# Optimization experiments

Hardware: AMD Instinct MI355X
Metric: run time of the kernel (lower is better)

Reference implementation:

```python
import jax, jax.numpy as jnp
import numpy as np

EPS = 1e-8
MIN_VAL = -1e7  # module default min_val=-10000000.0


def _div_safe(n, d):
    return n / jnp.maximum(d, EPS)


def _cosine_pairwise(v1, v2):
    # v1: (B,L1,H), v2: (B,L2,H) -> (B,L1,L2)
    n1 = jnp.linalg.norm(v1, axis=2, keepdims=True)
    n2 = jnp.linalg.norm(v2, axis=2, keepdims=True)
    a = jnp.einsum('bik,bjk->bij', v1, v2)
    return _div_safe(a, n1 * jnp.swapaxes(n2, 1, 2))


def _masked_max(v, mask, axis, keepdims=False):
    rep = jnp.where(mask > 0, v, MIN_VAL)
    val = jnp.max(rep, axis=axis, keepdims=keepdims)
    m = jnp.max(jnp.broadcast_to(mask, v.shape), axis=axis, keepdims=keepdims)
    return val * m


def _masked_mean(v, mask, axis, keepdims=False):
    s = jnp.sum(v * mask, axis=axis, keepdims=keepdims)
    c = jnp.sum(jnp.broadcast_to(mask, v.shape), axis=axis, keepdims=keepdims)
    return _div_safe(s, c)


def _cos_sim(a, b, axis):
    # torch F.cosine_similarity semantics: dot / (max(|a|,eps)*max(|b|,eps))
    dot = jnp.sum(a * b, axis=axis)
    na = jnp.maximum(jnp.linalg.norm(a, axis=axis), EPS)
    nb = jnp.maximum(jnp.linalg.norm(b, axis=axis), EPS)
    return dot / (na * nb)


def _mpm(v1, v2, w):
    # v1, v2: (B,L,H); w: (P,H) -> ((B,L,1), (B,L,P))
    mv1 = _cos_sim(v1, v2, 2)[..., None]
    v1w = w[None, None] * v1[:, :, None, :]  # (B,L,P,H)
    v2w = w[None, None] * v2[:, :, None, :]
    return mv1, _cos_sim(v1w, v2w, 3)


def _mpm_pairwise(v1, v2, w):
    # v1: (B,L1,H), v2: (B,L2,H), w: (P,H) -> (B,L1,L2,P)
    v1w = w[None, :, None, :] * v1[:, None, :, :]  # (B,P,L1,H)
    v2w = w[None, :, None, :] * v2[:, None, :, :]  # (B,P,L2,H)
    n1 = jnp.linalg.norm(v1w, axis=3, keepdims=True)
    n2 = jnp.linalg.norm(v2w, axis=3, keepdims=True)
    n = jnp.einsum('bpik,bpjk->bpij', v1w, v2w)
    d = n1 * jnp.swapaxes(n2, 2, 3)
    return jnp.transpose(_div_safe(n, d), (0, 2, 3, 1))


def setup_inputs() -> dict:
    key = jax.random.key(0)
    ks = jax.random.split(key, 8)
    B, L, H, P = 32, 128, 100, 20
    return {
        'context_p': jax.random.normal(ks[0], (B, L, H), dtype=jnp.float32),
        'mask_p': jax.random.randint(ks[1], (B, L), 0, 2, dtype=jnp.int32),
        'context_h': jax.random.normal(ks[2], (B, L, H), dtype=jnp.float32),
        'mask_h': jax.random.randint(ks[3], (B, L), 0, 2, dtype=jnp.int32),
        'w0': jax.random.uniform(ks[4], (P, H), dtype=jnp.float32),
        'w1': jax.random.uniform(ks[5], (P, H), dtype=jnp.float32),
        'w2': jax.random.uniform(ks[6], (P, H), dtype=jnp.float32),
        'w3': jax.random.uniform(ks[7], (P, H), dtype=jnp.float32),
    }


def reference(context_p, mask_p, context_h, mask_h, w0, w1, w2, w3):
    mask_p = mask_p.astype(jnp.float32)
    mask_h = mask_h.astype(jnp.float32)
    B, Lp, H = context_p.shape
    Lh = context_h.shape[1]

    mask_p_h = mask_p[:, :, None] * mask_h[:, None, :]   # (B,Lp,Lh)
    mask_h_p = jnp.swapaxes(mask_p_h, 1, 2)              # (B,Lh,Lp)
    cp = context_p * mask_p[..., None]
    ch = context_h * mask_h[..., None]

    # --- pairwise cosine + masked max/mean pooling ---
    cos = _cosine_pairwise(cp, ch)                        # (B,Lp,Lh)
    cosT = jnp.swapaxes(cos, 1, 2)
    cos_max_p = _masked_max(cos, mask_p_h, 2, True)
    cos_mean_p = _masked_mean(cos, mask_p_h, 2, True)
    cos_max_h = _masked_max(cosT, mask_h_p, 2, True)
    cos_mean_h = _masked_mean(cosT, mask_h_p, 2, True)

    # --- full match (is_forward=True: last real token) ---
    idx_p = jnp.clip(jnp.sum(mask_p, 1).astype(jnp.int32) - 1, 0)[:, None, None]
    idx_h = jnp.clip(jnp.sum(mask_h, 1).astype(jnp.int32) - 1, 0)[:, None, None]
    cp_last = jnp.take_along_axis(cp, jnp.broadcast_to(idx_p, (B, 1, H)), axis=1)
    ch_last = jnp.take_along_axis(ch, jnp.broadcast_to(idx_h, (B, 1, H)), axis=1)
    mv_p_f1, mv_p_fP = _mpm(cp, jnp.broadcast_to(ch_last, (B, Lp, H)), w0)
    mv_h_f1, mv_h_fP = _mpm(ch, jnp.broadcast_to(cp_last, (B, Lh, H)), w0)

    # --- maxpool match ---
    mv_max = _mpm_pairwise(cp, ch, w1)                    # (B,Lp,Lh,P)
    mv_p_max = _masked_max(mv_max, mask_p_h[..., None], 2)
    mv_p_mean = _masked_mean(mv_max, mask_p_h[..., None], 2)
    mv_maxT = jnp.transpose(mv_max, (0, 2, 1, 3))
    mv_h_max = _masked_max(mv_maxT, mask_h_p[..., None], 2)
    mv_h_mean = _masked_mean(mv_maxT, mask_h_p[..., None], 2)

    # --- attentive match (mean) ---
    att_mean_h = _div_safe(jnp.einsum('bij,bjh->bih', cos, ch),
                           jnp.sum(cos, 2, keepdims=True))
    att_mean_p = _div_safe(jnp.einsum('bij,bih->bjh', cos, cp),
                           jnp.swapaxes(jnp.sum(cos, 1, keepdims=True), 1, 2))
    mv_p_am1, mv_p_amP = _mpm(cp, att_mean_h, w2)
    mv_h_am1, mv_h_amP = _mpm(ch, att_mean_p, w2)

    # --- max-attentive match ---
    att_h = ch[:, None, :, :] * cos[:, :, :, None]        # (B,Lp,Lh,H)
    att_p_t = cp[:, None, :, :] * cosT[:, :, :, None]     # (B,Lh,Lp,H) == att_p.permute(0,2,1,3)
    att_max_h = _masked_max(att_h, mask_p_h[..., None], 2)
    att_max_p = _masked_max(att_p_t, mask_h_p[..., None], 2)
    mv_p_ax1, mv_p_axP = _mpm(cp, att_max_h, w3)
    mv_h_ax1, mv_h_axP = _mpm(ch, att_max_p, w3)

    mv_p = jnp.concatenate([cos_max_p, cos_mean_p, mv_p_f1, mv_p_fP,
                            mv_p_max, mv_p_mean, mv_p_am1, mv_p_amP,
                            mv_p_ax1, mv_p_axP], axis=2)
    mv_h = jnp.concatenate([cos_max_h, cos_mean_h, mv_h_f1, mv_h_fP,
                            mv_h_max, mv_h_mean, mv_h_am1, mv_h_amP,
                            mv_h_ax1, mv_h_axP], axis=2)
    return mv_p, mv_h
```

## Files before the change

### kernel.cpp

```cpp
#include <hip/hip_runtime.h>
#include <math.h>


namespace {
constexpr int B = 32;
constexpr int L = 128;
constexpr int H = 100;
constexpr int P = 20;
constexpr int C = 105;
constexpr int TI = 8;
constexpr float EPSF = 1e-8f;
constexpr float MINV = -1e7f;
}

typedef unsigned short u16;
typedef unsigned int u32;
typedef short sh8 __attribute__((ext_vector_type(8)));
typedef float f4 __attribute__((ext_vector_type(4)));

__device__ __forceinline__ u16 f2bf(float f) {
    u32 u = __float_as_uint(f);
    u += 0x7FFFu + ((u >> 16) & 1u);
    return (u16)(u >> 16);
}
__device__ __forceinline__ float bf2f(u32 h) {
    return __uint_as_float(h << 16);
}

__global__ void k_prep(const float* __restrict__ ctx_p, const int* __restrict__ mask_p,
                       const float* __restrict__ ctx_h, const int* __restrict__ mask_h,
                       const float* __restrict__ w1,
                       float* __restrict__ cp, float* __restrict__ ch,
                       u16* __restrict__ cpb, u16* __restrict__ chb,
                       float* __restrict__ np_, float* __restrict__ nh_,
                       float* __restrict__ nwp, float* __restrict__ nwh)
{
    const int b = blockIdx.y, i = blockIdx.x, side = blockIdx.z, t = threadIdx.x;
    const float* ctx = side ? ctx_h : ctx_p;
    const int*  mask = side ? mask_h : mask_p;
    float* dst  = side ? ch  : cp;
    u16*   dstb = side ? chb : cpb;
    float* nrm  = side ? nh_ : np_;
    float* nw   = side ? nwh : nwp;

    const int row = b * L + i;
    __shared__ __align__(16) float sv2[H];
    const float m = (float)mask[row];
    float v = 0.f;
    if (t < H) {
        v = ctx[row * H + t] * m;
        dst[row * H + t] = v;
        sv2[t] = v * v;
    }
    dstb[row * 128 + t] = f2bf(v);
    __syncthreads();

    const int w = t >> 6, ln = t & 63;
    int g = -1, seg = 0;
    if (w == 0) { if (ln < 60) { g = ln / 5; seg = ln % 5; } }
    else        { if (ln < 45) { g = 12 + ln / 5; seg = ln % 5; } }
    if (g >= 0) {
        const float4* v4 = (const float4*)sv2;
        float acc = 0.f;
        if (g < P) {
            const float4* w4 = (const float4*)(w1 + g * H);
            #pragma unroll
            for (int k = seg * 5; k < seg * 5 + 5; ++k) {
                float4 wv_ = w4[k], s = v4[k];
                acc += wv_.x * wv_.x * s.x + wv_.y * wv_.y * s.y +
                       wv_.z * wv_.z * s.z + wv_.w * wv_.w * s.w;
            }
        } else {
            #pragma unroll
            for (int k = seg * 5; k < seg * 5 + 5; ++k) {
                float4 s = v4[k];
                acc += s.x + s.y + s.z + s.w;
            }
        }
        float a1 = __shfl(acc, ln + 1), a2 = __shfl(acc, ln + 2);
        float a3 = __shfl(acc, ln + 3), a4 = __shfl(acc, ln + 4);
        if (seg == 0) {
            float s = acc + a1 + a2 + a3 + a4;
            if (g < P) nw[row * P + g] = sqrtf(s);
            else       nrm[row] = sqrtf(s);
        }
    }
}

__global__ __launch_bounds__(256) void
k_pair_mfma(const u16* __restrict__ Ab, const u16* __restrict__ Bb,
            const float* __restrict__ w1,
            const float* __restrict__ nwA, const float* __restrict__ nwB,
            const float* __restrict__ np_, const float* __restrict__ nh_,
            const int* __restrict__ maskA, const int* __restrict__ maskB,
            float* __restrict__ outP, float* __restrict__ outH,
            float* __restrict__ cosM, float* __restrict__ cosT,
            float* __restrict__ scP, float* __restrict__ scH)
{
    const int p = blockIdx.x, b = blockIdx.y, t = threadIdx.x;
    const bool is_cos = (p == P);
    __shared__ __align__(16) u16 sB[128 * 136];
    __shared__ float snwA[128], snwB[128], smA[128], smB[128];
    __shared__ float pJmax[128], pJsum[128], pJall[128];
    __shared__ float pImax[4][128], pIsum[4][128], pIall[4][128];
    __shared__ float sRed[4];

    if (t < 128) {
        snwA[t] = is_cos ? np_[b * L + t] : nwA[(b * L + t) * P + p];
        snwB[t] = is_cos ? nh_[b * L + t] : nwB[(b * L + t) * P + p];
        smA[t] = (float)maskA[b * L + t];
        smB[t] = (float)maskB[b * L + t];
    }
    __syncthreads();

    if (t < 64) {
        float a0 = smB[t], a1 = smB[t + 64];
        float mx = fmaxf(a0, a1), sm = a0 + a1;
        for (int d = 1; d < 64; d <<= 1) {
            mx = fmaxf(mx, __shfl_xor(mx, d));
            sm += __shfl_xor(sm, d);
        }
        if (t == 0) { sRed[2] = mx; sRed[3] = sm; }
    } else if (t < 128) {
        const int l = t - 64;
        float a0 = smA[l], a1 = smA[l + 64];
        float mx = fmaxf(a0, a1), sm = a0 + a1;
        for (int d = 1; d < 64; d <<= 1) {
            mx = fmaxf(mx, __shfl_xor(mx, d));
            sm += __shfl_xor(sm, d);
        }
        if (l == 0) { sRed[0] = mx; sRed[1] = sm; }
    }

    {
        const uint4* src = (const uint4*)(Bb + (size_t)b * L * 128);
        #pragma unroll
        for (int it = 0; it < 8; ++it) {
            int idx = it * 256 + t;
            int row = idx >> 4, kc = (idx & 15) * 8;
            uint4 v = src[idx];
            *(uint4*)&sB[row * 136 + kc] = v;
        }
    }
    __syncthreads();

    const int wave = t >> 6, lane = t & 63;
    const int m = lane & 15, q = lane >> 4;

    float swv[4][8];
    #pragma unroll
    for (int ks = 0; ks < 4; ++ks)
        #pragma unroll
        for (int e = 0; e < 8; ++e) {
            int k = ks * 32 + q * 8 + e;
            if (is_cos) swv[ks][e] = (k < H) ? 1.f : 0.f;
            else {
                float w = (k < H) ? w1[p * H + k] : 0.f;
                swv[ks][e] = w * w;
            }
        }

    f4 acc[2][8];
    #pragma unroll
    for (int rt = 0; rt < 2; ++rt)
        #pragma unroll
        for (int ct = 0; ct < 8; ++ct)
            acc[rt][ct] = (f4){0.f, 0.f, 0.f, 0.f};

    const uint4* gA0 = (const uint4*)(Ab + (size_t)(b * L + wave * 32 + m) * 128);
    const uint4* gA1 = (const uint4*)(Ab + (size_t)(b * L + wave * 32 + 16 + m) * 128);

    #pragma unroll
    for (int ks = 0; ks < 4; ++ks) {
        uint4 va0 = gA0[ks * 4 + q];
        uint4 va1 = gA1[ks * 4 + q];
        sh8 a0, a1;
        {
            u32 vs0[4] = {va0.x, va0.y, va0.z, va0.w};
            u32 vs1[4] = {va1.x, va1.y, va1.z, va1.w};
            u32 r0[4], r1[4];
            #pragma unroll
            for (int e = 0; e < 4; ++e) {
                float f0 = bf2f(vs0[e] & 0xffffu) * swv[ks][2 * e];
                float f1 = bf2f(vs0[e] >> 16) * swv[ks][2 * e + 1];
                r0[e] = (u32)f2bf(f0) | ((u32)f2bf(f1) << 16);
                float g0 = bf2f(vs1[e] & 0xffffu) * swv[ks][2 * e];
                float g1 = bf2f(vs1[e] >> 16) * swv[ks][2 * e + 1];
                r1[e] = (u32)f2bf(g0) | ((u32)f2bf(g1) << 16);
            }
            uint4 o0 = {r0[0], r0[1], r0[2], r0[3]};
            uint4 o1 = {r1[0], r1[1], r1[2], r1[3]};
            a0 = __builtin_bit_cast(sh8, o0);
            a1 = __builtin_bit_cast(sh8, o1);
        }
        const int ko = ks * 32 + q * 8;
        #pragma unroll
        for (int ct = 0; ct < 8; ++ct) {
            sh8 bb = *(const sh8*)&sB[(ct * 16 + m) * 136 + ko];
            acc[0][ct] = __builtin_amdgcn_mfma_f32_16x16x32_bf16(a0, bb, acc[0][ct], 0, 0, 0);
            acc[1][ct] = __builtin_amdgcn_mfma_f32_16x16x32_bf16(a1, bb, acc[1][ct], 0, 0, 0);
        }
    }

    float nB[8], mBv[8], imax[8], isum[8], iall[8];
    #pragma unroll
    for (int ct = 0; ct < 8; ++ct) {
        const int j = ct * 16 + m;
        nB[ct] = snwB[j]; mBv[ct] = smB[j];
        imax[ct] = MINV; isum[ct] = 0.f; iall[ct] = 0.f;
    }
    #pragma unroll
    for (int rt = 0; rt < 2; ++rt) {
        #pragma unroll
        for (int reg = 0; reg < 4; ++reg) {
            const int i = wave * 32 + rt * 16 + q * 4 + reg;
            const float na = snwA[i];
            const float ma = smA[i];
            float jmax = MINV, jsum = 0.f, jall = 0.f;
            #pragma unroll
            for (int ct = 0; ct < 8; ++ct) {
                float v = acc[rt][ct][reg] *
                          __builtin_amdgcn_rcpf(fmaxf(na * nB[ct], EPSF));
                if (is_cos) {
                    const int j = ct * 16 + m;
                    cosM[((size_t)b * L + i) * L + j] = v;
                    cosT[((size_t)b * L + j) * L + i] = v;
                    jall += v;
                    iall[ct] += v;
                }
                jmax = fmaxf(jmax, mBv[ct] > 0.f ? v : MINV);
                jsum += mBv[ct] > 0.f ? v : 0.f;
                imax[ct] = fmaxf(imax[ct], ma > 0.f ? v : MINV);
                isum[ct] += ma > 0.f ? v : 0.f;
            }
            for (int d = 1; d < 16; d <<= 1) {
                jmax = fmaxf(jmax, __shfl_xor(jmax, d));
                jsum += __shfl_xor(jsum, d);
                if (is_cos) jall += __shfl_xor(jall, d);
            }
            if (m == 0) { pJmax[i] = jmax; pJsum[i] = jsum; if (is_cos) pJall[i] = jall; }
        }
    }
    #pragma unroll
    for (int ct = 0; ct < 8; ++ct) {
        float mx = imax[ct], sm = isum[ct], al = iall[ct];
        mx = fmaxf(mx, __shfl_xor(mx, 16)); sm += __shfl_xor(sm, 16);
        mx = fmaxf(mx, __shfl_xor(mx, 32)); sm += __shfl_xor(sm, 32);
        if (is_cos) { al += __shfl_xor(al, 16); al += __shfl_xor(al, 32); }
        if (q == 0) {
            const int j = ct * 16 + m;
            pImax[wave][j] = mx; pIsum[wave][j] = sm;
            if (is_cos) pIall[wave][j] = al;
        }
    }
    __syncthreads();

    if (t < 128) {
        const int i = t;
        const int co0 = is_cos ? 0 : 23 + p;
        const int co1 = is_cos ? 1 : 43 + p;
        const float ma = smA[i];
        const float mm = ma * sRed[2];
        const float cnt = ma * sRed[3];
        float* orow = outP + ((size_t)b * L + i) * C;
        orow[co0] = pJmax[i] * mm;
        orow[co1] = ma * pJsum[i] / fmaxf(cnt, EPSF);

        const float mb = smB[i];
        const float hmax = fmaxf(fmaxf(pImax[0][i], pImax[1][i]),
                                 fmaxf(pImax[2][i], pImax[3][i]));
        const float hsum = pIsum[0][i] + pIsum[1][i] + pIsum[2][i] + pIsum[3][i];
        float* hrow = outH + ((size_t)b * L + i) * C;
        hrow[co0] = hmax * mb * sRed[0];
        hrow[co1] = mb * hsum / fmaxf(mb * sRed[1], EPSF);

        if (is_cos) {
            scP[b * L + i] = pJall[i];
            scH[b * L + i] = pIall[0][i] + pIall[1][i] + pIall[2][i] + pIall[3][i];
        }
    }
}

__global__ __launch_bounds__(256, 3) void
k_side_t(const float* __restrict__ cp, const float* __restrict__ ch,
         const u16* __restrict__ cpb, const u16* __restrict__ chb,
         const float* __restrict__ cosM, const float* __restrict__ cosT,
         const float* __restrict__ scP, const float* __restrict__ scH,
         const int* __restrict__ mask_p, const int* __restrict__ mask_h,
         const float* __restrict__ w0, const float* __restrict__ w2,
         const float* __restrict__ w3, float* __restrict__ out)
{
    const int tile = blockIdx.x, b = blockIdx.y, side = blockIdx.z, t = threadIdx.x;
    const int i0 = tile * TI;
    const float* A   = side ? ch : cp;
    const float* Bv  = side ? cp : ch;
    const u16*  Bvb  = side ? cpb : chb;
    const int* maskA = side ? mask_h : mask_p;
    const int* maskB = side ? mask_p : mask_h;
    const float* cosSrc = side ? cosT : cosM;
    const float* scArr  = side ? scH : scP;
    float* outBase = out + ((size_t)side * B * L + (size_t)b * L) * C;

    __shared__ __align__(16) u16  sBvC[128 * 128];
    __shared__ float scosC[TI][128];
    __shared__ __align__(16) float sa[TI][H];
    __shared__ __align__(16) float sam[TI][H];
    __shared__ __align__(16) float sax[TI][H];
    __shared__ __align__(16) float sl[H];
    __shared__ u16 cidx[128];
    __shared__ int snv;

    const int wv = t >> 6, ln = t & 63;

    if (wv == 0) {
        int m0 = maskB[b * L + ln], m1 = maskB[b * L + 64 + ln];
        unsigned long long b0 = __ballot(m0 > 0);
        unsigned long long b1 = __ballot(m1 > 0);
        unsigned long long pre = (1ull << ln) - 1ull;
        int n0 = __popcll(b0);
        if (m0 > 0) cidx[__popcll(b0 & pre)] = (u16)ln;
        if (m1 > 0) cidx[n0 + __popcll(b1 & pre)] = (u16)(64 + ln);
        if (ln == 0) snv = n0 + __popcll(b1);
    } else if (wv >= 2) {
        for (int x = t - 128; x < TI * 128; x += 128) {
            int il = x >> 7, k = x & 127;
            if (k < H) sa[il][k] = A[((size_t)b * L + i0 + il) * H + k];
        }
    }
    __syncthreads();
    const int nv = snv;

    {
        const uint4* src = (const uint4*)(Bvb + (size_t)b * L * 128);
        uint4* dst = (uint4*)sBvC;
        for (int c = t; c < nv * 16; c += 256) {
            int jj = c >> 4, cc = c & 15;
            dst[c] = src[(int)cidx[jj] * 16 + cc];
        }
        for (int x = t; x < TI * 128; x += 256) {
            int il = x >> 7, jj = x & 127;
            if (jj < nv)
                scosC[il][jj] = cosSrc[((size_t)b * L + i0 + il) * L + cidx[jj]];
        }
        if (wv == 1) {
            int last = nv - 1; if (last < 0) last = 0;
            const float* lr = Bv + ((size_t)b * L + last) * H;
            sl[ln] = lr[ln];
            if (ln + 64 < H) sl[ln + 64] = lr[ln + 64];
        }
    }
    __syncthreads();

    #pragma unroll
    for (int pass = 0; pass < 2; ++pass) {
        const int il = wv + pass * 4;
        const int gi = i0 + il;
        if (ln < 50) {
            const float mA = (float)maskA[b * L + gi];
            const float sc = scArr[b * L + gi];
            float am0 = 0.f, am1 = 0.f, ax0 = MINV, ax1 = MINV;
            const u32* bp = (const u32*)sBvC + ln;
            const float* cr = scosC[il];
            #pragma unroll 4
            for (int jj = 0; jj < nv; ++jj) {
                u32 pk = bp[jj * 64];
                float cj = cr[jj];
                float v0 = cj * __uint_as_float(pk << 16);
                float v1 = cj * __uint_as_float(pk & 0xffff0000u);
                am0 += v0; am1 += v1;
                ax0 = fmaxf(ax0, v0); ax1 = fmaxf(ax1, v1);
            }
            const float rs = __builtin_amdgcn_rcpf(fmaxf(sc, EPSF));
            const float mm = (nv > 0) ? mA : 0.f;
            sam[il][2 * ln] = am0 * rs; sam[il][2 * ln + 1] = am1 * rs;
            sax[il][2 * ln] = ax0 * mm; sax[il][2 * ln + 1] = ax1 * mm;
        }
    }
    __syncthreads();

    for (int task = t; task < TI * 63; task += 256) {
        const int il = task / 63, c = task - il * 63;
        float* orow = outBase + (size_t)(i0 + il) * C;
        const float4* a4 = (const float4*)sa[il];
        if (c < 60) {
            const int grp = c / 20, p = c - grp * 20;
            const float* wrow = (grp == 0 ? w0 : grp == 1 ? w2 : w3) + p * H;
            const float* oth = grp == 0 ? sl : grp == 1 ? sam[il] : sax[il];
            const float4* w4 = (const float4*)wrow;
            const float4* o4 = (const float4*)oth;
            float d = 0.f, na = 0.f, nb = 0.f;
            #pragma unroll 5
            for (int k = 0; k < H / 4; ++k) {
                float4 w = w4[k], a = a4[k], o = o4[k];
                float ww;
                ww = w.x * w.x; d += ww * a.x * o.x; na += ww * a.x * a.x; nb += ww * o.x * o.x;
                ww = w.y * w.y; d += ww * a.y * o.y; na += ww * a.y * a.y; nb += ww * o.y * o.y;
                ww = w.z * w.z; d += ww * a.z * o.z; na += ww * a.z * a.z; nb += ww * o.z * o.z;
                ww = w.w * w.w; d += ww * a.w * o.w; na += ww * a.w * a.w; nb += ww * o.w * o.w;
            }
            const int base = (grp == 0) ? 3 : (grp == 1) ? 64 : 85;
            orow[base + p] = d / (fmaxf(sqrtf(na), EPSF) * fmaxf(sqrtf(nb), EPSF));
        } else {
            const float* oth = (c == 60) ? sl : (c == 61) ? sam[il] : sax[il];
            const float4* o4 = (const float4*)oth;
            float d = 0.f, na = 0.f, nb = 0.f;
            #pragma unroll 5
            for (int k = 0; k < H / 4; ++k) {
                float4 a = a4[k], o = o4[k];
                d += a.x * o.x + a.y * o.y + a.z * o.z + a.w * o.w;
                na += a.x * a.x + a.y * a.y + a.z * a.z + a.w * a.w;
                nb += o.x * o.x + o.y * o.y + o.z * o.z + o.w * o.w;
            }
            orow[(c == 60) ? 2 : (c == 61) ? 63 : 84] =
                d / (fmaxf(sqrtf(na), EPSF) * fmaxf(sqrtf(nb), EPSF));
        }
    }
}

extern "C" void kernel_launch(void* const* d_in, const int* in_sizes, int n_in,
                              void* d_out, int out_size, void* d_ws, size_t ws_size,
                              hipStream_t stream)
{
    const float* ctx_p = (const float*)d_in[0];
    const int*   mask_p = (const int*)d_in[1];
    const float* ctx_h = (const float*)d_in[2];
    const int*   mask_h = (const int*)d_in[3];
    const float* w0 = (const float*)d_in[4];
    const float* w1 = (const float*)d_in[5];
    const float* w2 = (const float*)d_in[6];
    const float* w3 = (const float*)d_in[7];
    float* out = (float*)d_out;

    float* ws   = (float*)d_ws;
    float* cp   = ws;
    float* ch   = cp   + B * L * H;
    float* np_  = ch   + B * L * H;
    float* nh_  = np_  + B * L;
    float* nw1p = nh_  + B * L;
    float* nw1h = nw1p + B * L * P;
    float* cosM = nw1h + B * L * P;
    float* cosT = cosM + B * L * L;
    float* scP  = cosT + B * L * L;
    float* scH  = scP  + B * L;
    u16*   cpb  = (u16*)(scH + B * L);
    u16*   chb  = cpb + B * L * 128;

    float* out_h = out + B * L * C;

    k_prep<<<dim3(L, B, 2), dim3(128), 0, stream>>>(
        ctx_p, mask_p, ctx_h, mask_h, w1,
        cp, ch, cpb, chb, np_, nh_, nw1p, nw1h);
    k_pair_mfma<<<dim3(P + 1, B), dim3(256), 0, stream>>>(
        cpb, chb, w1, nw1p, nw1h, np_, nh_, mask_p, mask_h,
        out, out_h, cosM, cosT, scP, scH);
    k_side_t<<<dim3(L / TI, B, 2), dim3(256), 0, stream>>>(
        cp, ch, cpb, chb, cosM, cosT, scP, scH,
        mask_p, mask_h, w0, w2, w3, out);
}
```

Before: 138.9 us.

## Fuse pairwise MFMA and side-attention kernels, recompute cosine tiles locally with masked compaction

```diff
diff --git a/kernel.cpp b/kernel.cpp
--- a/kernel.cpp
+++ b/kernel.cpp
@@ -9,6 +9,7 @@
 constexpr int P = 20;
 constexpr int C = 105;
 constexpr int TI = 8;
+constexpr int SMEM_BYTES = 50176;
 constexpr float EPSF = 1e-8f;
 constexpr float MINV = -1e7f;
 }
@@ -88,331 +89,358 @@
 }
 
 __global__ __launch_bounds__(256) void
-k_pair_mfma(const u16* __restrict__ Ab, const u16* __restrict__ Bb,
-            const float* __restrict__ w1,
-            const float* __restrict__ nwA, const float* __restrict__ nwB,
-            const float* __restrict__ np_, const float* __restrict__ nh_,
-            const int* __restrict__ maskA, const int* __restrict__ maskB,
-            float* __restrict__ outP, float* __restrict__ outH,
-            float* __restrict__ cosM, float* __restrict__ cosT,
-            float* __restrict__ scP, float* __restrict__ scH)
+k_main(const float* __restrict__ cp, const float* __restrict__ ch,
+       const u16* __restrict__ cpb, const u16* __restrict__ chb,
+       const float* __restrict__ np_, const float* __restrict__ nh_,
+       const float* __restrict__ nw1p, const float* __restrict__ nw1h,
+       const int* __restrict__ mask_p, const int* __restrict__ mask_h,
+       const float* __restrict__ w0, const float* __restrict__ w1,
+       const float* __restrict__ w2, const float* __restrict__ w3,
+       float* __restrict__ out)
 {
-    const int p = blockIdx.x, b = blockIdx.y, t = threadIdx.x;
-    const bool is_cos = (p == P);
-    __shared__ __align__(16) u16 sB[128 * 136];
-    __shared__ float snwA[128], snwB[128], smA[128], smB[128];
-    __shared__ float pJmax[128], pJsum[128], pJall[128];
-    __shared__ float pImax[4][128], pIsum[4][128], pIall[4][128];
-    __shared__ float sRed[4];
-
-    if (t < 128) {
-        snwA[t] = is_cos ? np_[b * L + t] : nwA[(b * L + t) * P + p];
-        snwB[t] = is_cos ? nh_[b * L + t] : nwB[(b * L + t) * P + p];
-        smA[t] = (float)maskA[b * L + t];
-        smB[t] = (float)maskB[b * L + t];
-    }
-    __syncthreads();
-
-    if (t < 64) {
-        float a0 = smB[t], a1 = smB[t + 64];
-        float mx = fmaxf(a0, a1), sm = a0 + a1;
-        for (int d = 1; d < 64; d <<= 1) {
-            mx = fmaxf(mx, __shfl_xor(mx, d));
-            sm += __shfl_xor(sm, d);
-        }
-        if (t == 0) { sRed[2] = mx; sRed[3] = sm; }
-    } else if (t < 128) {
-        const int l = t - 64;
-        float a0 = smA[l], a1 = smA[l + 64];
-        float mx = fmaxf(a0, a1), sm = a0 + a1;
-        for (int d = 1; d < 64; d <<= 1) {
-            mx = fmaxf(mx, __shfl_xor(mx, d));
-            sm += __shfl_xor(sm, d);
-        }
-        if (l == 0) { sRed[0] = mx; sRed[1] = sm; }
-    }
-
-    {
-        const uint4* src = (const uint4*)(Bb + (size_t)b * L * 128);
-        #pragma unroll
-        for (int it = 0; it < 8; ++it) {
-            int idx = it * 256 + t;
-            int row = idx >> 4, kc = (idx & 15) * 8;
-            uint4 v = src[idx];
-            *(uint4*)&sB[row * 136 + kc] = v;
-        }
-    }
-    __syncthreads();
-
-    const int wave = t >> 6, lane = t & 63;
-    const int m = lane & 15, q = lane >> 4;
-
-    float swv[4][8];
-    #pragma unroll
-    for (int ks = 0; ks < 4; ++ks)
-        #pragma unroll
-        for (int e = 0; e < 8; ++e) {
-            int k = ks * 32 + q * 8 + e;
-            if (is_cos) swv[ks][e] = (k < H) ? 1.f : 0.f;
-            else {
+    __shared__ __align__(16) char smem[SMEM_BYTES];
+    const int bx = blockIdx.x, b = blockIdx.y, t = threadIdx.x;
+    const int wv = t >> 6, ln = t & 63;
+    float* out_p = out;
+    float* out_h = out + (size_t)B * L * C;
+
+    if (bx < P) {
+        const int p = bx;
+        u16*  sB    = (u16*)smem;
+        float* snwA = (float*)(smem + 34816);
+        float* snwB = (float*)(smem + 35328);
+        float* smA  = (float*)(smem + 35840);
+        float* smB  = (float*)(smem + 36352);
+        float* pJmax= (float*)(smem + 36864);
+        float* pJsum= (float*)(smem + 37376);
+        float* pImax= (float*)(smem + 37888);
+        float* pIsum= (float*)(smem + 39936);
+        float* sRed = (float*)(smem + 41984);
+
+        if (t < 128) {
+            snwA[t] = nw1p[(b * L + t) * P + p];
+            snwB[t] = nw1h[(b * L + t) * P + p];
+            smA[t] = (float)mask_p[b * L + t];
+            smB[t] = (float)mask_h[b * L + t];
+        }
+        __syncthreads();
+
+        if (t < 64) {
+            float a0 = smB[t], a1 = smB[t + 64];
+            float mx = fmaxf(a0, a1), sm = a0 + a1;
+            for (int d = 1; d < 64; d <<= 1) {
+                mx = fmaxf(mx, __shfl_xor(mx, d));
+                sm += __shfl_xor(sm, d);
+            }
+            if (t == 0) { sRed[2] = mx; sRed[3] = sm; }
+        } else if (t < 128) {
+            const int l = t - 64;
+            float a0 = smA[l], a1 = smA[l + 64];
+            float mx = fmaxf(a0, a1), sm = a0 + a1;
+            for (int d = 1; d < 64; d <<= 1) {
+                mx = fmaxf(mx, __shfl_xor(mx, d));
+                sm += __shfl_xor(sm, d);
+            }
+            if (l == 0) { sRed[0] = mx; sRed[1] = sm; }
+        }
+
+        {
+            const uint4* src = (const uint4*)(chb + (size_t)b * L * 128);
+            #pragma unroll
+            for (int it = 0; it < 8; ++it) {
+                int idx = it * 256 + t;
+                int row = idx >> 4, kc = (idx & 15) * 8;
+                uint4 v = src[idx];
+                *(uint4*)&sB[row * 136 + kc] = v;
+            }
+        }
+        __syncthreads();
+
+        const int m = ln & 15, q = ln >> 4;
+
+        float swv[4][8];
+        #pragma unroll
+        for (int ks = 0; ks < 4; ++ks)
+            #pragma unroll
+            for (int e = 0; e < 8; ++e) {
+                int k = ks * 32 + q * 8 + e;
                 float w = (k < H) ? w1[p * H + k] : 0.f;
                 swv[ks][e] = w * w;
             }
-        }
-
-    f4 acc[2][8];
-    #pragma unroll
-    for (int rt = 0; rt < 2; ++rt)
-        #pragma unroll
-        for (int ct = 0; ct < 8; ++ct)
-            acc[rt][ct] = (f4){0.f, 0.f, 0.f, 0.f};
-
-    const uint4* gA0 = (const uint4*)(Ab + (size_t)(b * L + wave * 32 + m) * 128);
-    const uint4* gA1 = (const uint4*)(Ab + (size_t)(b * L + wave * 32 + 16 + m) * 128);
-
-    #pragma unroll
-    for (int ks = 0; ks < 4; ++ks) {
-        uint4 va0 = gA0[ks * 4 + q];
-        uint4 va1 = gA1[ks * 4 + q];
-        sh8 a0, a1;
+
+        f4 acc[2][8];
+        #pragma unroll
+        for (int rt = 0; rt < 2; ++rt)
+            #pragma unroll
+            for (int ct = 0; ct < 8; ++ct)
+                acc[rt][ct] = (f4){0.f, 0.f, 0.f, 0.f};
+
+        const uint4* gA0 = (const uint4*)(cpb + (size_t)(b * L + wv * 32 + m) * 128);
+        const uint4* gA1 = (const uint4*)(cpb + (size_t)(b * L + wv * 32 + 16 + m) * 128);
+
+        #pragma unroll
+        for (int ks = 0; ks < 4; ++ks) {
+            uint4 va0 = gA0[ks * 4 + q];
+            uint4 va1 = gA1[ks * 4 + q];
+            sh8 a0, a1;
+            {
+                u32 vs0[4] = {va0.x, va0.y, va0.z, va0.w};
+                u32 vs1[4] = {va1.x, va1.y, va1.z, va1.w};
+                u32 r0[4], r1[4];
+                #pragma unroll
+                for (int e = 0; e < 4; ++e) {
+                    float f0 = bf2f(vs0[e] & 0xffffu) * swv[ks][2 * e];
+                    float f1 = bf2f(vs0[e] >> 16) * swv[ks][2 * e + 1];
+                    r0[e] = (u32)f2bf(f0) | ((u32)f2bf(f1) << 16);
+                    float g0 = bf2f(vs1[e] & 0xffffu) * swv[ks][2 * e];
+                    float g1 = bf2f(vs1[e] >> 16) * swv[ks][2 * e + 1];
+                    r1[e] = (u32)f2bf(g0) | ((u32)f2bf(g1) << 16);
+                }
+                uint4 o0 = {r0[0], r0[1], r0[2], r0[3]};
+                uint4 o1 = {r1[0], r1[1], r1[2], r1[3]};
+                a0 = __builtin_bit_cast(sh8, o0);
+                a1 = __builtin_bit_cast(sh8, o1);
+            }
+            const int ko = ks * 32 + q * 8;
+            #pragma unroll
+            for (int ct = 0; ct < 8; ++ct) {
+                sh8 bb = *(const sh8*)&sB[(ct * 16 + m) * 136 + ko];
+                acc[0][ct] = __builtin_amdgcn_mfma_f32_16x16x32_bf16(a0, bb, acc[0][ct], 0, 0, 0);
+                acc[1][ct] = __builtin_amdgcn_mfma_f32_16x16x32_bf16(a1, bb, acc[1][ct], 0, 0, 0);
+            }
+        }
+
+        float nB[8], mBv[8], imax[8], isum[8];
+        #pragma unroll
+        for (int ct = 0; ct < 8; ++ct) {
+            const int j = ct * 16 + m;
+            nB[ct] = snwB[j]; mBv[ct] = smB[j];
+            imax[ct] = MINV; isum[ct] = 0.f;
+        }
+        #pragma unroll
+        for (int rt = 0; rt < 2; ++rt) {
+            #pragma unroll
+            for (int reg = 0; reg < 4; ++reg) {
+                const int i = wv * 32 + rt * 16 + q * 4 + reg;
+                const float na = snwA[i];
+                const float ma = smA[i];
+                float jmax = MINV, jsum = 0.f;
+                #pragma unroll
+                for (int ct = 0; ct < 8; ++ct) {
+                    float v = acc[rt][ct][reg] *
+                              __builtin_amdgcn_rcpf(fmaxf(na * nB[ct], EPSF));
+                    jmax = fmaxf(jmax, mBv[ct] > 0.f ? v : MINV);
+                    jsum += mBv[ct] > 0.f ? v : 0.f;
+                    imax[ct] = fmaxf(imax[ct], ma > 0.f ? v : MINV);
+                    isum[ct] += ma > 0.f ? v : 0.f;
+                }
+                for (int d = 1; d < 16; d <<= 1) {
+                    jmax = fmaxf(jmax, __shfl_xor(jmax, d));
+                    jsum += __shfl_xor(jsum, d);
+                }
+                if (m == 0) { pJmax[i] = jmax; pJsum[i] = jsum; }
+            }
+        }
+        #pragma unroll
+        for (int ct = 0; ct < 8; ++ct) {
+            float mx = imax[ct], sm = isum[ct];
+            mx = fmaxf(mx, __shfl_xor(mx, 16)); sm += __shfl_xor(sm, 16);
+            mx = fmaxf(mx, __shfl_xor(mx, 32)); sm += __shfl_xor(sm, 32);
+            if (q == 0) { const int j = ct * 16 + m; pImax[wv * 128 + j] = mx; pIsum[wv * 128 + j] = sm; }
+        }
+        __syncthreads();
+
+        if (t < 128) {
+            const int i = t;
+            const float ma = smA[i];
+            const float mm = ma * sRed[2];
+            const float cnt = ma * sRed[3];
+            float* orow = out_p + ((size_t)b * L + i) * C;
+            orow[23 + p] = pJmax[i] * mm;
+            orow[43 + p] = ma * pJsum[i] / fmaxf(cnt, EPSF);
+
+            const float mb = smB[i];
+            const float hmax = fmaxf(fmaxf(pImax[0 * 128 + i], pImax[1 * 128 + i]),
+                                     fmaxf(pImax[2 * 128 + i], pImax[3 * 128 + i]));
+            const float hsum = pIsum[0 * 128 + i] + pIsum[1 * 128 + i] +
+                               pIsum[2 * 128 + i] + pIsum[3 * 128 + i];
+            float* hrow = out_h + ((size_t)b * L + i) * C;
+            hrow[23 + p] = hmax * mb * sRed[0];
+            hrow[43 + p] = mb * hsum / fmaxf(mb * sRed[1], EPSF);
+        }
+    } else {
+        const int e = bx - P;
+        const int side = e >> 4, tile = e & 15;
+        const int i0 = tile * TI;
+        const float* A   = side ? ch : cp;
+        const float* Bv  = side ? cp : ch;
+        const u16*  Ab16 = side ? chb : cpb;
+        const u16*  Bvb  = side ? cpb : chb;
+        const float* nA_ = side ? nh_ : np_;
+        const float* nB_ = side ? np_ : nh_;
+        const int* maskA = side ? mask_h : mask_p;
+        const int* maskB = side ? mask_p : mask_h;
+        float* outBase = out + ((size_t)side * B * L + (size_t)b * L) * C;
+
+        float* scosC = (float*)(smem + 34816);
+        float* sa    = (float*)(smem + 38912);
+        float* sam   = (float*)(smem + 42112);
+        float* sax   = (float*)(smem + 45312);
+        float* sl    = (float*)(smem + 48512);
+        float* snB   = (float*)(smem + 48912);
+        u16*  cidx  = (u16*)(smem + 49424);
+        float* snA   = (float*)(smem + 49680);
+        int*   pnv   = (int*)(smem + 49712);
+
+        if (wv == 0) {
+            int m0 = maskB[b * L + ln], m1 = maskB[b * L + 64 + ln];
+            unsigned long long b0 = __ballot(m0 > 0);
+            unsigned long long b1 = __ballot(m1 > 0);
+            unsigned long long pre = (1ull << ln) - 1ull;
+            int n0 = __popcll(b0);
+            if (m0 > 0) cidx[__popcll(b0 & pre)] = (u16)ln;
+            if (m1 > 0) cidx[n0 + __popcll(b1 & pre)] = (u16)(64 + ln);
+            if (ln == 0) *pnv = n0 + __popcll(b1);
+        } else if (wv >= 2) {
+            for (int x = t - 128; x < TI * 128; x += 128) {
+                int il = x >> 7, k = x & 127;
+                if (k < H) sa[il * 100 + k] = A[((size_t)b * L + i0 + il) * H + k];
+            }
+        }
+        __syncthreads();
+        const int nv = *pnv;
+        const int nct = (nv + 15) >> 4;
+
         {
-            u32 vs0[4] = {va0.x, va0.y, va0.z, va0.w};
-            u32 vs1[4] = {va1.x, va1.y, va1.z, va1.w};
-            u32 r0[4], r1[4];
-            #pragma unroll
-            for (int e = 0; e < 4; ++e) {
-                float f0 = bf2f(vs0[e] & 0xffffu) * swv[ks][2 * e];
-                float f1 = bf2f(vs0[e] >> 16) * swv[ks][2 * e + 1];
-                r0[e] = (u32)f2bf(f0) | ((u32)f2bf(f1) << 16);
-                float g0 = bf2f(vs1[e] & 0xffffu) * swv[ks][2 * e];
-                float g1 = bf2f(vs1[e] >> 16) * swv[ks][2 * e + 1];
-                r1[e] = (u32)f2bf(g0) | ((u32)f2bf(g1) << 16);
-            }
-            uint4 o0 = {r0[0], r0[1], r0[2], r0[3]};
-            uint4 o1 = {r1[0], r1[1], r1[2], r1[3]};
-            a0 = __builtin_bit_cast(sh8, o0);
-            a1 = __builtin_bit_cast(sh8, o1);
-        }
-        const int ko = ks * 32 + q * 8;
-        #pragma unroll
-        for (int ct = 0; ct < 8; ++ct) {
-            sh8 bb = *(const sh8*)&sB[(ct * 16 + m) * 136 + ko];
-            acc[0][ct] = __builtin_amdgcn_mfma_f32_16x16x32_bf16(a0, bb, acc[0][ct], 0, 0, 0);
-            acc[1][ct] = __builtin_amdgcn_mfma_f32_16x16x32_bf16(a1, bb, acc[1][ct], 0, 0, 0);
-        }
-    }
-
-    float nB[8], mBv[8], imax[8], isum[8], iall[8];
-    #pragma unroll
-    for (int ct = 0; ct < 8; ++ct) {
-        const int j = ct * 16 + m;
-        nB[ct] = snwB[j]; mBv[ct] = smB[j];
-        imax[ct] = MINV; isum[ct] = 0.f; iall[ct] = 0.f;
-    }
-    #pragma unroll
-    for (int rt = 0; rt < 2; ++rt) {
-        #pragma unroll
-        for (int reg = 0; reg < 4; ++reg) {
-            const int i = wave * 32 + rt * 16 + q * 4 + reg;
-            const float na = snwA[i];
-            const float ma = smA[i];
-            float jmax = MINV, jsum = 0.f, jall = 0.f;
-            #pragma unroll
-            for (int ct = 0; ct < 8; ++ct) {
-                float v = acc[rt][ct][reg] *
-                          __builtin_amdgcn_rcpf(fmaxf(na * nB[ct], EPSF));
-                if (is_cos) {
-                    const int j = ct * 16 + m;
-                    cosM[((size_t)b * L + i) * L + j] = v;
-                    cosT[((size_t)b * L + j) * L + i] = v;
-                    jall += v;
-                    iall[ct] += v;
-                }
-                jmax = fmaxf(jmax, mBv[ct] > 0.f ? v : MINV);
-                jsum += mBv[ct] > 0.f ? v : 0.f;
-                imax[ct] = fmaxf(imax[ct], ma > 0.f ? v : MINV);
-                isum[ct] += ma > 0.f ? v : 0.f;
-            }
-            for (int d = 1; d < 16; d <<= 1) {
-                jmax = fmaxf(jmax, __shfl_xor(jmax, d));
-                jsum += __shfl_xor(jsum, d);
-                if (is_cos) jall += __shfl_xor(jall, d);
-            }
-            if (m == 0) { pJmax[i] = jmax; pJsum[i] = jsum; if (is_cos) pJall[i] = jall; }
-        }
-    }
-    #pragma unroll
-    for (int ct = 0; ct < 8; ++ct) {
-        float mx = imax[ct], sm = isum[ct], al = iall[ct];
-        mx = fmaxf(mx, __shfl_xor(mx, 16)); sm += __shfl_xor(sm, 16);
-        mx = fmaxf(mx, __shfl_xor(mx, 32)); sm += __shfl_xor(sm, 32);
-        if (is_cos) { al += __shfl_xor(al, 16); al += __shfl_xor(al, 32); }
-        if (q == 0) {
-            const int j = ct * 16 + m;
-            pImax[wave][j] = mx; pIsum[wave][j] = sm;
-            if (is_cos) pIall[wave][j] = al;
-        }
-    }
-    __syncthreads();
-
-    if (t < 128) {
-        const int i = t;
-        const int co0 = is_cos ? 0 : 23 + p;
-        const int co1 = is_cos ? 1 : 43 + p;
-        const float ma = smA[i];
-        const float mm = ma * sRed[2];
-        const float cnt = ma * sRed[3];
-        float* orow = outP + ((size_t)b * L + i) * C;
-        orow[co0] = pJmax[i] * mm;
-        orow[co1] = ma * pJsum[i] / fmaxf(cnt, EPSF);
-
-        const float mb = smB[i];
-        const float hmax = fmaxf(fmaxf(pImax[0][i], pImax[1][i]),
-                                 fmaxf(pImax[2][i], pImax[3][i]));
-        const float hsum = pIsum[0][i] + pIsum[1][i] + pIsum[2][i] + pIsum[3][i];
-        float* hrow = outH + ((size_t)b * L + i) * C;
-        hrow[co0] = hmax * mb * sRed[0];
-        hrow[co1] = mb * hsum / fmaxf(mb * sRed[1], EPSF);
-
-        if (is_cos) {
-            scP[b * L + i] = pJall[i];
-            scH[b * L + i] = pIall[0][i] + pIall[1][i] + pIall[2][i] + pIall[3][i];
-        }
-    }
-}
-
-__global__ __launch_bounds__(256, 3) void
-k_side_t(const float* __restrict__ cp, const float* __restrict__ ch,
-         const u16* __restrict__ cpb, const u16* __restrict__ chb,
-         const float* __restrict__ cosM, const float* __restrict__ cosT,
-         const float* __restrict__ scP, const float* __restrict__ scH,
-         const int* __restrict__ mask_p, const int* __restrict__ mask_h,
-         const float* __restrict__ w0, const float* __restrict__ w2,
-         const float* __restrict__ w3, float* __restrict__ out)
-{
-    const int tile = blockIdx.x, b = blockIdx.y, side = blockIdx.z, t = threadIdx.x;
-    const int i0 = tile * TI;
-    const float* A   = side ? ch : cp;
-    const float* Bv  = side ? cp : ch;
-    const u16*  Bvb  = side ? cpb : chb;
-    const int* maskA = side ? mask_h : mask_p;
-    const int* maskB = side ? mask_p : mask_h;
-    const float* cosSrc = side ? cosT : cosM;
-    const float* scArr  = side ? scH : scP;
-    float* outBase = out + ((size_t)side * B * L + (size_t)b * L) * C;
-
-    __shared__ __align__(16) u16  sBvC[128 * 128];
-    __shared__ float scosC[TI][128];
-    __shared__ __align__(16) float sa[TI][H];
-    __shared__ __align__(16) float sam[TI][H];
-    __shared__ __align__(16) float sax[TI][H];
-    __shared__ __align__(16) float sl[H];
-    __shared__ u16 cidx[128];
-    __shared__ int snv;
-
-    const int wv = t >> 6, ln = t & 63;
-
-    if (wv == 0) {
-        int m0 = maskB[b * L + ln], m1 = maskB[b * L + 64 + ln];
-        unsigned long long b0 = __ballot(m0 > 0);
-        unsigned long long b1 = __ballot(m1 > 0);
-        unsigned long long pre = (1ull << ln) - 1ull;
-        int n0 = __popcll(b0);
-        if (m0 > 0) cidx[__popcll(b0 & pre)] = (u16)ln;
-        if (m1 > 0) cidx[n0 + __popcll(b1 & pre)] = (u16)(64 + ln);
-        if (ln == 0) snv = n0 + __popcll(b1);
-    } else if (wv >= 2) {
-        for (int x = t - 128; x < TI * 128; x += 128) {
-            int il = x >> 7, k = x & 127;
-            if (k < H) sa[il][k] = A[((size_t)b * L + i0 + il) * H + k];
-        }
-    }
-    __syncthreads();
-    const int nv = snv;
-
-    {
-        const uint4* src = (const uint4*)(Bvb + (size_t)b * L * 128);
-        uint4* dst = (uint4*)sBvC;
-        for (int c = t; c < nv * 16; c += 256) {
-            int jj = c >> 4, cc = c & 15;
-            dst[c] = src[(int)cidx[jj] * 16 + cc];
-        }
-        for (int x = t; x < TI * 128; x += 256) {
-            int il = x >> 7, jj = x & 127;
-            if (jj < nv)
-                scosC[il][jj] = cosSrc[((size_t)b * L + i0 + il) * L + cidx[jj]];
-        }
-        if (wv == 1) {
-            int last = nv - 1; if (last < 0) last = 0;
-            const float* lr = Bv + ((size_t)b * L + last) * H;
-            sl[ln] = lr[ln];
-            if (ln + 64 < H) sl[ln + 64] = lr[ln + 64];
-        }
-    }
-    __syncthreads();
-
-    #pragma unroll
-    for (int pass = 0; pass < 2; ++pass) {
-        const int il = wv + pass * 4;
-        const int gi = i0 + il;
-        if (ln < 50) {
-            const float mA = (float)maskA[b * L + gi];
-            const float sc = scArr[b * L + gi];
-            float am0 = 0.f, am1 = 0.f, ax0 = MINV, ax1 = MINV;
-            const u32* bp = (const u32*)sBvC + ln;
-            const float* cr = scosC[il];
-            #pragma unroll 4
-            for (int jj = 0; jj < nv; ++jj) {
-                u32 pk = bp[jj * 64];
-                float cj = cr[jj];
-                float v0 = cj * __uint_as_float(pk << 16);
-                float v1 = cj * __uint_as_float(pk & 0xffff0000u);
-                am0 += v0; am1 += v1;
-                ax0 = fmaxf(ax0, v0); ax1 = fmaxf(ax1, v1);
-            }
-            const float rs = __builtin_amdgcn_rcpf(fmaxf(sc, EPSF));
-            const float mm = (nv > 0) ? mA : 0.f;
-            sam[il][2 * ln] = am0 * rs; sam[il][2 * ln + 1] = am1 * rs;
-            sax[il][2 * ln] = ax0 * mm; sax[il][2 * ln + 1] = ax1 * mm;
-        }
-    }
-    __syncthreads();
-
-    for (int task = t; task < TI * 63; task += 256) {
-        const int il = task / 63, c = task - il * 63;
-        float* orow = outBase + (size_t)(i0 + il) * C;
-        const float4* a4 = (const float4*)sa[il];
-        if (c < 60) {
-            const int grp = c / 20, p = c - grp * 20;
-            const float* wrow = (grp == 0 ? w0 : grp == 1 ? w2 : w3) + p * H;
-            const float* oth = grp == 0 ? sl : grp == 1 ? sam[il] : sax[il];
-            const float4* w4 = (const float4*)wrow;
-            const float4* o4 = (const float4*)oth;
-            float d = 0.f, na = 0.f, nb = 0.f;
-            #pragma unroll 5
-            for (int k = 0; k < H / 4; ++k) {
-                float4 w = w4[k], a = a4[k], o = o4[k];
-                float ww;
-                ww = w.x * w.x; d += ww * a.x * o.x; na += ww * a.x * a.x; nb += ww * o.x * o.x;
-                ww = w.y * w.y; d += ww * a.y * o.y; na += ww * a.y * a.y; nb += ww * o.y * o.y;
-                ww = w.z * w.z; d += ww * a.z * o.z; na += ww * a.z * a.z; nb += ww * o.z * o.z;
-                ww = w.w * w.w; d += ww * a.w * o.w; na += ww * a.w * a.w; nb += ww * o.w * o.w;
-            }
-            const int base = (grp == 0) ? 3 : (grp == 1) ? 64 : 85;
-            orow[base + p] = d / (fmaxf(sqrtf(na), EPSF) * fmaxf(sqrtf(nb), EPSF));
-        } else {
-            const float* oth = (c == 60) ? sl : (c == 61) ? sam[il] : sax[il];
-            const float4* o4 = (const float4*)oth;
-            float d = 0.f, na = 0.f, nb = 0.f;
-            #pragma unroll 5
-            for (int k = 0; k < H / 4; ++k) {
-                float4 a = a4[k], o = o4[k];
-                d += a.x * o.x + a.y * o.y + a.z * o.z + a.w * o.w;
-                na += a.x * a.x + a.y * a.y + a.z * a.z + a.w * a.w;
-                nb += o.x * o.x + o.y * o.y + o.z * o.z + o.w * o.w;
-            }
-            orow[(c == 60) ? 2 : (c == 61) ? 63 : 84] =
-                d / (fmaxf(sqrtf(na), EPSF) * fmaxf(sqrtf(nb), EPSF));
+            const uint4* src = (const uint4*)(Bvb + (size_t)b * L * 128);
+            for (int c = t; c < nct * 256; c += 256) {
+                int jj = c >> 4, cc = c & 15;
+                uint4 v;
+                if (jj < nv) v = src[(int)cidx[jj] * 16 + cc];
+                else { v.x = v.y = v.z = v.w = 0u; }
+                *(uint4*)(smem + jj * 272 + cc * 16) = v;
+            }
+            if (t < 128) snB[t] = (t < nv) ? nB_[b * L + (int)cidx[t]] : 0.f;
+            else if (t < 136) snA[t - 128] = nA_[b * L + i0 + (t - 128)];
+            if (wv == 1) {
+                int last = nv - 1; if (last < 0) last = 0;
+                const float* lr = Bv + ((size_t)b * L + last) * H;
+                sl[ln] = lr[ln];
+                if (ln + 64 < H) sl[ln + 64] = lr[ln + 64];
+            }
+        }
+        __syncthreads();
+
+        const int m = ln & 15, q = ln >> 4;
+        {
+            const uint4* gA = (const uint4*)(Ab16 + (size_t)(b * L + i0 + (m & 7)) * 128);
+            f4 acc0 = (f4){0.f, 0.f, 0.f, 0.f};
+            f4 acc1 = (f4){0.f, 0.f, 0.f, 0.f};
+            const int ct0 = wv, ct1 = wv + 4;
+            #pragma unroll
+            for (int ks = 0; ks < 4; ++ks) {
+                uint4 va = gA[ks * 4 + q];
+                if (m >= 8) { va.x = va.y = va.z = va.w = 0u; }
+                sh8 af = __builtin_bit_cast(sh8, va);
+                const int ko2 = (ks * 32 + q * 8) * 2;
+                if (ct0 < nct) {
+                    sh8 bb = *(const sh8*)(smem + (ct0 * 16 + m) * 272 + ko2);
+                    acc0 = __builtin_amdgcn_mfma_f32_16x16x32_bf16(af, bb, acc0, 0, 0, 0);
+                }
+                if (ct1 < nct) {
+                    sh8 bb = *(const sh8*)(smem + (ct1 * 16 + m) * 272 + ko2);
+                    acc1 = __builtin_amdgcn_mfma_f32_16x16x32_bf16(af, bb, acc1, 0, 0, 0);
+                }
+            }
+            if (q < 2) {
+                #pragma unroll
+                for (int reg = 0; reg < 4; ++reg) {
+                    const int i = q * 4 + reg;
+                    const float ni = snA[i];
+                    if (ct0 < nct) {
+                        const int jj = ct0 * 16 + m;
+                        scosC[i * 128 + jj] = acc0[reg] *
+                            __builtin_amdgcn_rcpf(fmaxf(ni * snB[jj], EPSF));
+                    }
+                    if (ct1 < nct) {
+                        const int jj = ct1 * 16 + m;
+                        scosC[i * 128 + jj] = acc1[reg] *
+                            __builtin_amdgcn_rcpf(fmaxf(ni * snB[jj], EPSF));
+                    }
+                }
+            }
+        }
+        __syncthreads();
+
+        #pragma unroll
+        for (int pass = 0; pass < 2; ++pass) {
+            const int il = wv + pass * 4;
+            const int gi = i0 + il;
+            if (ln < 50) {
+                const float mA = (float)maskA[b * L + gi];
+                float am0 = 0.f, am1 = 0.f, ax0 = MINV, ax1 = MINV;
+                float scj = 0.f, cmx = MINV;
+                const u32* bp = (const u32*)smem + ln;
+                const float* cr = scosC + il * 128;
+                #pragma unroll 4
+                for (int jj = 0; jj < nv; ++jj) {
+                    u32 pk = bp[jj * 68];
+                    float cj = cr[jj];
+                    scj += cj; cmx = fmaxf(cmx, cj);
+                    float v0 = cj * __uint_as_float(pk << 16);
+                    float v1 = cj * __uint_as_float(pk & 0xffff0000u);
+                    am0 += v0; am1 += v1;
+                    ax0 = fmaxf(ax0, v0); ax1 = fmaxf(ax1, v1);
+                }
+                const float rs = __builtin_amdgcn_rcpf(fmaxf(scj, EPSF));
+                const float mm = (nv > 0) ? mA : 0.f;
+                sam[il * 100 + 2 * ln] = am0 * rs; sam[il * 100 + 2 * ln + 1] = am1 * rs;
+                sax[il * 100 + 2 * ln] = ax0 * mm; sax[il * 100 + 2 * ln + 1] = ax1 * mm;
+                if (ln == 0) {
+                    float* orow = outBase + (size_t)gi * C;
+                    orow[0] = cmx * mm;
+                    orow[1] = mA * scj / fmaxf(mA * (float)nv, EPSF);
+                }
+            }
+        }
+        __syncthreads();
+
+        for (int task = t; task < TI * 63; task += 256) {
+            const int il = task / 63, c = task - il * 63;
+            float* orow = outBase + (size_t)(i0 + il) * C;
+            const float4* a4 = (const float4*)(sa + il * 100);
+            if (c < 60) {
+                const int grp = c / 20, p = c - grp * 20;
+                const float* wrow = (grp == 0 ? w0 : grp == 1 ? w2 : w3) + p * H;
+                const float* oth = grp == 0 ? sl : (grp == 1 ? sam : sax) + il * 100;
+                const float4* w4 = (const float4*)wrow;
+                const float4* o4 = (const float4*)oth;
+                float d = 0.f, na = 0.f, nb = 0.f;
+                #pragma unroll 5
+                for (int k = 0; k < H / 4; ++k) {
+                    float4 w = w4[k], a = a4[k], o = o4[k];
+                    float ww;
+                    ww = w.x * w.x; d += ww * a.x * o.x; na += ww * a.x * a.x; nb += ww * o.x * o.x;
+                    ww = w.y * w.y; d += ww * a.y * o.y; na += ww * a.y * a.y; nb += ww * o.y * o.y;
+                    ww = w.z * w.z; d += ww * a.z * o.z; na += ww * a.z * a.z; nb += ww * o.z * o.z;
+                    ww = w.w * w.w; d += ww * a.w * o.w; na += ww * a.w * a.w; nb += ww * o.w * o.w;
+                }
+                const int base = (grp == 0) ? 3 : (grp == 1) ? 64 : 85;
+                orow[base + p] = d / (fmaxf(sqrtf(na), EPSF) * fmaxf(sqrtf(nb), EPSF));
+            } else {
+                const float* oth = (c == 60) ? sl : ((c == 61) ? sam : sax) + il * 100;
+                const float4* o4 = (const float4*)oth;
+                float d = 0.f, na = 0.f, nb = 0.f;
+                #pragma unroll 5
+                for (int k = 0; k < H / 4; ++k) {
+                    float4 a = a4[k], o = o4[k];
+                    d += a.x * o.x + a.y * o.y + a.z * o.z + a.w * o.w;
+                    na += a.x * a.x + a.y * a.y + a.z * a.z + a.w * a.w;
+                    nb += o.x * o.x + o.y * o.y + o.z * o.z + o.w * o.w;
+                }
+                orow[(c == 60) ? 2 : (c == 61) ? 63 : 84] =
+                    d / (fmaxf(sqrtf(na), EPSF) * fmaxf(sqrtf(nb), EPSF));
+            }
         }
     }
 }
@@ -438,22 +466,13 @@
     float* nh_  = np_  + B * L;
     float* nw1p = nh_  + B * L;
     float* nw1h = nw1p + B * L * P;
-    float* cosM = nw1h + B * L * P;
-    float* cosT = cosM + B * L * L;
-    float* scP  = cosT + B * L * L;
-    float* scH  = scP  + B * L;
-    u16*   cpb  = (u16*)(scH + B * L);
+    u16*   cpb  = (u16*)(nw1h + B * L * P);
     u16*   chb  = cpb + B * L * 128;
-
-    float* out_h = out + B * L * C;
 
     k_prep<<<dim3(L, B, 2), dim3(128), 0, stream>>>(
         ctx_p, mask_p, ctx_h, mask_h, w1,
         cp, ch, cpb, chb, np_, nh_, nw1p, nw1h);
-    k_pair_mfma<<<dim3(P + 1, B), dim3(256), 0, stream>>>(
-        cpb, chb, w1, nw1p, nw1h, np_, nh_, mask_p, mask_h,
-        out, out_h, cosM, cosT, scP, scH);
-    k_side_t<<<dim3(L / TI, B, 2), dim3(256), 0, stream>>>(
-        cp, ch, cpb, chb, cosM, cosT, scP, scH,
-        mask_p, mask_h, w0, w2, w3, out);
-}
+    k_main<<<dim3(P + 32, B), dim3(256), 0, stream>>>(
+        cp, ch, cpb, chb, np_, nh_, nw1p, nw1h, mask_p, mask_h,
+        w0, w1, w2, w3, out);
+}
```

Result: no change. 136.7 us (-1.6%).
